# Optimization experiments

Hardware: AMD Instinct MI355X
Metric: run time of the kernel (lower is better)

## Reference

```python
import jax, jax.numpy as jnp
import numpy as np

LATENT_DIM = 8
HALF = LATENT_DIM // 2
N_BLOCKS = 3
EPS = 1e-10


def _causal_graphs(koopman):
    # koopman: [C, D, D] real. Batched eig-decomp, band-pass eigenvalues by |lam| in [0.9, 1.1],
    # equivalent to selecting stable columns/rows: V_s diag(lam_s) V_s^-1 == V diag(lam*mask) V^-1.
    lam, V = jnp.linalg.eig(koopman)            # lam: [C,D] complex, V: [C,D,D]
    Vinv = jnp.linalg.inv(V)
    lam = lam + (1e-10 + 1e-10j)
    a = jnp.abs(lam)
    mask = (a <= 1.1) & (a >= 0.9)              # [C,D]
    # fallback: if no stable eigenvalue in a group, keep all (torch.arange branch)
    mask = jnp.where(jnp.any(mask, axis=-1, keepdims=True), mask, True)
    lam_m = lam * mask.astype(lam.dtype)
    G = jnp.einsum('cij,cj,cjk->cik', V, lam_m, Vinv)
    return jnp.real(G).astype(koopman.dtype)    # [C,D,D]


def _coupling(x, cond, W0, b0, W1, b1, W2, b2):
    # Conditional affine coupling flow: x,cond [..., D]. Returns (z, logdet [...])
    logdet = jnp.zeros(x.shape[:-1], dtype=x.dtype)
    for i in range(N_BLOCKS):
        x1, x2 = x[..., :HALF], x[..., HALF:]
        if i % 2 == 1:
            x1, x2 = x2, x1
        h = jnp.concatenate([x1, cond], axis=-1)            # [..., HALF + D]
        h = jax.nn.relu(h @ W0[i] + b0[i])
        h = jax.nn.relu(h @ W1[i] + b1[i])
        o = h @ W2[i] + b2[i]                               # [..., 2*HALF]
        s = jnp.tanh(o[..., :HALF])
        t = o[..., HALF:]
        x2 = x2 * jnp.exp(s) + t
        logdet = logdet + jnp.sum(s, axis=-1)
        if i % 2 == 1:
            x1, x2 = x2, x1
        x = jnp.concatenate([x1, x2], axis=-1)
    return x, logdet


def _std_normal_logprob(z):
    # standard MVN log prob, summed over last dim
    D = z.shape[-1]
    c = jnp.asarray(0.5 * D * np.log(2.0 * np.pi), dtype=z.dtype)
    return -0.5 * jnp.sum(z * z, axis=-1) - c


def setup_inputs() -> dict:
    key = jax.random.key(0)
    ks = jax.random.split(key, 9)
    B, N, T, D, C, H = 32, 4096, 16, LATENT_DIM, 32, 64
    latent = jax.random.normal(ks[0], (B, N, T, D), dtype=jnp.float32)
    # scale so eigenvalue magnitudes cluster near ~1 (spectral radius of D x D gaussian ~ 0.35*sqrt(D))
    koopman_tilde = jax.random.normal(ks[1], (C, D, D), dtype=jnp.float32) * 0.35
    community = jax.random.normal(ks[2], (N, C), dtype=jnp.float32)
    s0 = 1.0 / np.sqrt(HALF + D)
    s1 = 1.0 / np.sqrt(H)
    W0 = jax.random.normal(ks[3], (N_BLOCKS, HALF + D, H), dtype=jnp.float32) * s0
    b0 = jnp.zeros((N_BLOCKS, H), dtype=jnp.float32)
    W1 = jax.random.normal(ks[4], (N_BLOCKS, H, H), dtype=jnp.float32) * s1
    b1 = jnp.zeros((N_BLOCKS, H), dtype=jnp.float32)
    W2 = jax.random.normal(ks[5], (N_BLOCKS, H, 2 * HALF), dtype=jnp.float32) * s1
    b2 = jnp.zeros((N_BLOCKS, 2 * HALF), dtype=jnp.float32)
    return {"latent": latent, "koopman_tilde": koopman_tilde, "community": community,
            "W0": W0, "b0": b0, "W1": W1, "b1": b1, "W2": W2, "b2": b2}


def reference(latent, koopman_tilde, community, W0, b0, W1, b1, W2, b2):
    # scale_type == 'community' branch
    community_class = jnp.argmax(community, axis=-1)        # [N], topk k=1 indices
    graphs = _causal_graphs(koopman_tilde)                  # [C, D, D]
    G_node = graphs[community_class]                        # [N, D, D] gather per node
    # dispatch/matmul/combine fused as one einsum (parent[:, class==i] = latent[:, class==i] @ G_i)
    parent = jnp.einsum('bntd,nde->bnte', latent, G_node)
    ez, logdet = _coupling(latent, parent, W0, b0, W1, b1, W2, b2)
    log_pz = _std_normal_logprob(ez) + logdet               # [B, N, T]
    return log_pz
```

## Files before the change

kernel.cpp:

```cpp
#include <hip/hip_runtime.h>
#include <hip/hip_bf16.h>

typedef __attribute__((ext_vector_type(8))) short     bf16x8;
typedef __attribute__((ext_vector_type(4))) float     f32x4;
typedef __attribute__((ext_vector_type(4))) unsigned  u32x4;

__device__ inline unsigned short bf16_rn(float x) {
  unsigned u = __float_as_uint(x);
  unsigned r = (u + 0x7FFFu + ((u >> 16) & 1u)) >> 16;
  return (unsigned short)r;
}
__device__ inline unsigned cvt_pk_bf16(float a, float b) {
  unsigned r;
  asm("v_cvt_pk_bf16_f32 %0, %1, %2" : "=v"(r) : "v"(a), "v"(b));
  return r;
}
__device__ inline void cbar() { asm volatile("" ::: "memory"); }
__device__ inline float tanh_fast(float v) {
  float vv = fminf(fmaxf(v, -15.f), 15.f);
  float e = __expf(2.f * vv);
  return (e - 1.f) * __frcp_rn(e + 1.f);
}

__global__ __launch_bounds__(256) void prologue_kernel(
    const float* __restrict__ Kt, const float* __restrict__ comm,
    const float* __restrict__ W0, const float* __restrict__ W1,
    const float* __restrict__ W2,
    float* __restrict__ Gout, int* __restrict__ cls,
    unsigned* __restrict__ wfrag)
{
  const int b = blockIdx.x;
  const int t = threadIdx.x;

  if (b < 32) {
    __shared__ double Kd[64];
    __shared__ double Pw[2][64];
    __shared__ double psum[8];
    __shared__ double coefs[9];
    __shared__ double rts[16];
    __shared__ double Gpart[64][8];

    const int tl = t & 63;
    const int row = tl >> 3, col = tl & 7;

    if (t < 64) Kd[tl] = (double)Kt[b * 64 + tl];
    __syncthreads();
    if (t < 64) Pw[0][tl] = Kd[tl];
    __syncthreads();

    int cur = 0;
    for (int p = 1; p <= 8; ++p) {
      if (t == 0) {
        double tr = 0.0;
        for (int d = 0; d < 8; ++d) tr += Pw[cur][d * 9];
        psum[p - 1] = tr;
      }
      if (p < 8 && t < 64) {
        double sacc = 0.0;
        for (int k = 0; k < 8; ++k) sacc += Pw[cur][row * 8 + k] * Kd[k * 8 + col];
        Pw[cur ^ 1][tl] = sacc;
      }
      __syncthreads();
      cur ^= 1;
    }

    if (t == 0) {
      double a[9];
      a[0] = 1.0;
      for (int k = 1; k <= 8; ++k) {
        double ssum = psum[k - 1];
        for (int i = 1; i < k; ++i) ssum += a[i] * psum[k - i - 1];
        a[k] = -ssum / (double)k;
      }
      for (int k = 0; k <= 8; ++k) coefs[k] = a[k];
    }
    __syncthreads();

    if (t < 8) {
      double a8[9];
      #pragma unroll
      for (int k = 0; k <= 8; ++k) a8[k] = coefs[k];
      double zre = 1.0, zim = 0.0;
      for (int q = 0; q <= t; ++q) {
        double t1 = zre * 0.4 - zim * 0.9;
        double t2 = zre * 0.9 + zim * 0.4;
        zre = t1; zim = t2;
      }
      for (int it = 0; it < 40; ++it) {
        double pre = a8[0], pim = 0.0;
        #pragma unroll
        for (int k = 1; k <= 8; ++k) {
          double t1 = pre * zre - pim * zim + a8[k];
          double t2 = pre * zim + pim * zre;
          pre = t1; pim = t2;
        }
        double dre = 1.0, dim = 0.0;
        for (int j = 0; j < 8; ++j) {
          double ore = __shfl(zre, j, 64);
          double oim = __shfl(zim, j, 64);
          if (j != t) {
            double sre = zre - ore, sim = zim - oim;
            double t1 = dre * sre - dim * sim;
            double t2 = dre * sim + dim * sre;
            dre = t1; dim = t2;
          }
        }
        double d2 = dre * dre + dim * dim;
        if (d2 < 1e-60) d2 = 1e-60;
        double qre = (pre * dre + pim * dim) / d2;
        double qim = (pim * dre - pre * dim) / d2;
        zre -= qre; zim -= qim;
      }
      rts[t] = zre; rts[8 + t] = zim;
    }
    __syncthreads();

    if (t < 64) {
      double lre[8], lim[8];
      #pragma unroll
      for (int j = 0; j < 8; ++j) { lre[j] = rts[j]; lim[j] = rts[8 + j]; }

      bool keep[8]; bool any = false;
      #pragma unroll
      for (int j = 0; j < 8; ++j) {
        double sre = lre[j] + 1e-10, sim = lim[j] + 1e-10;
        double amod = sqrt(sre * sre + sim * sim);
        keep[j] = (amod <= 1.1) && (amod >= 0.9);
        any = any || keep[j];
      }
      #pragma unroll
      for (int j = 0; j < 8; ++j) if (!any) keep[j] = true;

      const int r = tl >> 3, myrow = tl & 7;
      const int first = (r == 0) ? 1 : 0;
      double vre[8], vim[8];
      #pragma unroll
      for (int cc = 0; cc < 8; ++cc) {
        vre[cc] = Kd[myrow * 8 + cc] - ((myrow == cc) ? lre[first] : 0.0);
        vim[cc] = (myrow == cc) ? -lim[first] : 0.0;
      }
      #pragma unroll
      for (int j = 0; j < 8; ++j) {
        if (j == r || j == first) continue;
        double nre[8], nim[8];
        #pragma unroll
        for (int cc = 0; cc < 8; ++cc) {
          double are = 0.0, aim = 0.0;
          #pragma unroll
          for (int k = 0; k < 8; ++k) {
            double bre = Kd[k * 8 + cc] - ((k == cc) ? lre[j] : 0.0);
            double bim = (k == cc) ? -lim[j] : 0.0;
            are += vre[k] * bre - vim[k] * bim;
            aim += vre[k] * bim + vim[k] * bre;
          }
          nre[cc] = are; nim[cc] = aim;
        }
        #pragma unroll
        for (int cc = 0; cc < 8; ++cc) { vre[cc] = nre[cc]; vim[cc] = nim[cc]; }
      }

      double dre = 1.0, dim = 0.0;
      #pragma unroll
      for (int j = 0; j < 8; ++j) {
        if (j == r) continue;
        double ure = lre[r] - lre[j], uim = lim[r] - lim[j];
        double t1 = dre * ure - dim * uim;
        double t2 = dre * uim + dim * ure;
        dre = t1; dim = t2;
      }
      double numre = keep[r] ? (lre[r] + 1e-10) : 0.0;
      double numim = keep[r] ? (lim[r] + 1e-10) : 0.0;
      double dd = dre * dre + dim * dim;
      if (dd < 1e-300) dd = 1e-300;
      double cre = (numre * dre + numim * dim) / dd;
      double cim = (numim * dre - numre * dim) / dd;

      #pragma unroll
      for (int cc = 0; cc < 8; ++cc)
        Gpart[tl][cc] = cre * vre[cc] - cim * vim[cc];
    }
    __syncthreads();

    if (t < 64) {
      double sum = 0.0;
      #pragma unroll
      for (int rr = 0; rr < 8; ++rr) sum += Gpart[rr * 8 + (t >> 3)][t & 7];
      Gout[b * 64 + t] = (float)sum;
    }
    return;
  }

  if (b < 48) {
    int n = (b - 32) * 256 + t;
    if (n < 4096) {
      const float* rowp = comm + n * 32;
      float best = rowp[0];
      int bi = 0;
      #pragma unroll
      for (int c = 1; c < 32; ++c) {
        float v = rowp[c];
        if (v > best) { best = v; bi = c; }
      }
      cls[n] = bi;
    }
    return;
  }

  {
    int gid = (b - 48) * 256 + t;
    if (gid >= 42 * 64) return;
    int fid = gid >> 6, lane = gid & 63;
    int i = fid / 14, fl = fid % 14;
    int c = lane & 15, g = lane >> 4;

    unsigned short vals[8];
    #pragma unroll
    for (int j = 0; j < 8; ++j) {
      float v = 0.f;
      if (fl < 4) {
        int nb = fl;
        int k = 8 * g + j;
        if (k < 12) v = W0[i * 768 + k * 64 + 16 * nb + c];
      } else if (fl < 12) {
        int q = fl - 4; int kb = q >> 2, nb = q & 3;
        int k = 32 * kb + 16 * ((j >> 2) & 1) + 4 * g + 2 * ((j >> 1) & 1) + (j & 1);
        v = W1[i * 4096 + k * 64 + 16 * nb + c];
      } else {
        int kb = fl - 12;
        int k = 32 * kb + 16 * ((j >> 2) & 1) + 4 * g + 2 * ((j >> 1) & 1) + (j & 1);
        if (c < 8) v = W2[i * 512 + k * 8 + c];
      }
      vals[j] = bf16_rn(v);
    }
    u32x4 o;
    #pragma unroll
    for (int tt = 0; tt < 4; ++tt)
      o[tt] = (unsigned)vals[2 * tt] | ((unsigned)vals[2 * tt + 1] << 16);
    *(u32x4*)(wfrag + fid * 256 + lane * 4) = o;
  }
}

#define SPB 256

__global__ __launch_bounds__(256, 3) void causal_mfma_kernel(
    const float* __restrict__ latent, const float* __restrict__ graphs,
    const int* __restrict__ cls, const unsigned* __restrict__ wfrag,
    const float* __restrict__ b0, const float* __restrict__ b1,
    const float* __restrict__ b2, float* __restrict__ out)
{
  __shared__ char LW[4][4096];

  const int t = threadIdx.x;
  const int lane = t & 63;
  const int w = t >> 6;
  const int c = lane & 15;
  const int g = lane >> 4;
  const int s = blockIdx.x * SPB + t;
  char* my = LW[w];

  float x[8];
  {
    const float4 xa = *(const float4*)(latent + (size_t)s * 8);
    const float4 xb = *(const float4*)(latent + (size_t)s * 8 + 4);
    x[0] = xa.x; x[1] = xa.y; x[2] = xa.z; x[3] = xa.w;
    x[4] = xb.x; x[5] = xb.y; x[6] = xb.z; x[7] = xb.w;
  }
  unsigned parP0, parP1;
  u32x4 hi4;
  {
    float par[8];
    const int n = (s >> 4) & 4095;
    const float* G = graphs + cls[n] * 64;
    #pragma unroll
    for (int e = 0; e < 8; ++e) par[e] = 0.f;
    #pragma unroll
    for (int d = 0; d < 8; ++d) {
      const float xd = x[d];
      const float4 g0 = *(const float4*)(G + d * 8);
      const float4 g1 = *(const float4*)(G + d * 8 + 4);
      par[0] += xd * g0.x; par[1] += xd * g0.y; par[2] += xd * g0.z; par[3] += xd * g0.w;
      par[4] += xd * g1.x; par[5] += xd * g1.y; par[6] += xd * g1.z; par[7] += xd * g1.w;
    }
    parP0 = cvt_pk_bf16(par[0], par[1]);
    parP1 = cvt_pk_bf16(par[2], par[3]);
    hi4[0] = cvt_pk_bf16(par[4], par[5]);
    hi4[1] = cvt_pk_bf16(par[6], par[7]);
    hi4[2] = 0u; hi4[3] = 0u;
  }

  const int ssw = (lane >> 2) & 3;
  char* a_u0 = my + lane * 64 + ((0 ^ ssw) << 4);
  char* a_u1 = my + lane * 64 + ((1 ^ ssw) << 4);
  {
    const u32x4 z = {0u, 0u, 0u, 0u};
    *(u32x4*)(my + lane * 64 + ((2 ^ ssw) << 4)) = z;
    *(u32x4*)(my + lane * 64 + ((3 ^ ssw) << 4)) = z;
  }
  const int gsw = g ^ (c >> 2);
  char* a_b0 = my + (c)      * 64 + (gsw << 4);
  char* a_b1 = my + (16 + c) * 64 + (gsw << 4);
  char* a_b2 = my + (32 + c) * 64 + (gsw << 4);
  char* a_b3 = my + (48 + c) * 64 + (gsw << 4);

  float logdet = 0.f;

  #pragma unroll
  for (int i = 0; i < 3; ++i) {
    const int in0 = (i & 1) ? 4 : 0;
    const int tr0 = (i & 1) ? 0 : 4;
    const char* wbase = (const char*)wfrag + (size_t)(i * 14) * 1024 + lane * 16;

    {
      u32x4 lo4;
      lo4[0] = cvt_pk_bf16(x[in0], x[in0 + 1]);
      lo4[1] = cvt_pk_bf16(x[in0 + 2], x[in0 + 3]);
      lo4[2] = parP0; lo4[3] = parP1;
      *(u32x4*)a_u0 = lo4;
      *(u32x4*)a_u1 = hi4;
    }
    cbar();

    u32x4 B1[4];
    B1[0] = *(const u32x4*)a_b0;
    B1[1] = *(const u32x4*)a_b1;
    B1[2] = *(const u32x4*)a_b2;
    B1[3] = *(const u32x4*)a_b3;

    u32x4 B2k0[4], B2k1[4];
    {
      f32x4 a0[4], a1[4];
      bf16x8 A0 = *(const bf16x8*)(wbase + 0 * 1024);
      bf16x8 A1 = *(const bf16x8*)(wbase + 1 * 1024);
      f32x4 bv0 = *(const f32x4*)(b0 + i * 64 + 0 * 16 + g * 4);
      f32x4 bv1 = *(const f32x4*)(b0 + i * 64 + 1 * 16 + g * 4);
      #pragma unroll
      for (int mb = 0; mb < 4; ++mb)
        a0[mb] = __builtin_amdgcn_mfma_f32_16x16x32_bf16(
            A0, __builtin_bit_cast(bf16x8, B1[mb]), bv0, 0, 0, 0);
      #pragma unroll
      for (int mb = 0; mb < 4; ++mb)
        a1[mb] = __builtin_amdgcn_mfma_f32_16x16x32_bf16(
            A1, __builtin_bit_cast(bf16x8, B1[mb]), bv1, 0, 0, 0);
      #pragma unroll
      for (int mb = 0; mb < 4; ++mb) {
        B2k0[mb] = u32x4{cvt_pk_bf16(fmaxf(a0[mb][0], 0.f), fmaxf(a0[mb][1], 0.f)),
                         cvt_pk_bf16(fmaxf(a0[mb][2], 0.f), fmaxf(a0[mb][3], 0.f)),
                         cvt_pk_bf16(fmaxf(a1[mb][0], 0.f), fmaxf(a1[mb][1], 0.f)),
                         cvt_pk_bf16(fmaxf(a1[mb][2], 0.f), fmaxf(a1[mb][3], 0.f))};
      }
    }
    {
      f32x4 a0[4], a1[4];
      bf16x8 A0 = *(const bf16x8*)(wbase + 2 * 1024);
      bf16x8 A1 = *(const bf16x8*)(wbase + 3 * 1024);
      f32x4 bv0 = *(const f32x4*)(b0 + i * 64 + 2 * 16 + g * 4);
      f32x4 bv1 = *(const f32x4*)(b0 + i * 64 + 3 * 16 + g * 4);
      #pragma unroll
      for (int mb = 0; mb < 4; ++mb)
        a0[mb] = __builtin_amdgcn_mfma_f32_16x16x32_bf16(
            A0, __builtin_bit_cast(bf16x8, B1[mb]), bv0, 0, 0, 0);
      #pragma unroll
      for (int mb = 0; mb < 4; ++mb)
        a1[mb] = __builtin_amdgcn_mfma_f32_16x16x32_bf16(
            A1, __builtin_bit_cast(bf16x8, B1[mb]), bv1, 0, 0, 0);
      #pragma unroll
      for (int mb = 0; mb < 4; ++mb) {
        B2k1[mb] = u32x4{cvt_pk_bf16(fmaxf(a0[mb][0], 0.f), fmaxf(a0[mb][1], 0.f)),
                         cvt_pk_bf16(fmaxf(a0[mb][2], 0.f), fmaxf(a0[mb][3], 0.f)),
                         cvt_pk_bf16(fmaxf(a1[mb][0], 0.f), fmaxf(a1[mb][1], 0.f)),
                         cvt_pk_bf16(fmaxf(a1[mb][2], 0.f), fmaxf(a1[mb][3], 0.f))};
      }
    }

    u32x4 B3k0[4], B3k1[4];
    {
      f32x4 a0[4], a1[4];
      bf16x8 Ak0n0 = *(const bf16x8*)(wbase + (4 + 0) * 1024);
      bf16x8 Ak0n1 = *(const bf16x8*)(wbase + (4 + 1) * 1024);
      bf16x8 Ak1n0 = *(const bf16x8*)(wbase + (8 + 0) * 1024);
      bf16x8 Ak1n1 = *(const bf16x8*)(wbase + (8 + 1) * 1024);
      f32x4 bv0 = *(const f32x4*)(b1 + i * 64 + 0 * 16 + g * 4);
      f32x4 bv1 = *(const f32x4*)(b1 + i * 64 + 1 * 16 + g * 4);
      #pragma unroll
      for (int mb = 0; mb < 4; ++mb) {
        a0[mb] = __builtin_amdgcn_mfma_f32_16x16x32_bf16(
            Ak0n0, __builtin_bit_cast(bf16x8, B2k0[mb]), bv0, 0, 0, 0);
        a0[mb] = __builtin_amdgcn_mfma_f32_16x16x32_bf16(
            Ak1n0, __builtin_bit_cast(bf16x8, B2k1[mb]), a0[mb], 0, 0, 0);
      }
      #pragma unroll
      for (int mb = 0; mb < 4; ++mb) {
        a1[mb] = __builtin_amdgcn_mfma_f32_16x16x32_bf16(
            Ak0n1, __builtin_bit_cast(bf16x8, B2k0[mb]), bv1, 0, 0, 0);
        a1[mb] = __builtin_amdgcn_mfma_f32_16x16x32_bf16(
            Ak1n1, __builtin_bit_cast(bf16x8, B2k1[mb]), a1[mb], 0, 0, 0);
      }
      #pragma unroll
      for (int mb = 0; mb < 4; ++mb) {
        B3k0[mb] = u32x4{cvt_pk_bf16(fmaxf(a0[mb][0], 0.f), fmaxf(a0[mb][1], 0.f)),
                         cvt_pk_bf16(fmaxf(a0[mb][2], 0.f), fmaxf(a0[mb][3], 0.f)),
                         cvt_pk_bf16(fmaxf(a1[mb][0], 0.f), fmaxf(a1[mb][1], 0.f)),
                         cvt_pk_bf16(fmaxf(a1[mb][2], 0.f), fmaxf(a1[mb][3], 0.f))};
      }
    }
    {
      f32x4 a0[4], a1[4];
      bf16x8 Ak0n2 = *(const bf16x8*)(wbase + (4 + 2) * 1024);
      bf16x8 Ak0n3 = *(const bf16x8*)(wbase + (4 + 3) * 1024);
      bf16x8 Ak1n2 = *(const bf16x8*)(wbase + (8 + 2) * 1024);
      bf16x8 Ak1n3 = *(const bf16x8*)(wbase + (8 + 3) * 1024);
      f32x4 bv0 = *(const f32x4*)(b1 + i * 64 + 2 * 16 + g * 4);
      f32x4 bv1 = *(const f32x4*)(b1 + i * 64 + 3 * 16 + g * 4);
      #pragma unroll
      for (int mb = 0; mb < 4; ++mb) {
        a0[mb] = __builtin_amdgcn_mfma_f32_16x16x32_bf16(
            Ak0n2, __builtin_bit_cast(bf16x8, B2k0[mb]), bv0, 0, 0, 0);
        a0[mb] = __builtin_amdgcn_mfma_f32_16x16x32_bf16(
            Ak1n2, __builtin_bit_cast(bf16x8, B2k1[mb]), a0[mb], 0, 0, 0);
      }
      #pragma unroll
      for (int mb = 0; mb < 4; ++mb) {
        a1[mb] = __builtin_amdgcn_mfma_f32_16x16x32_bf16(
            Ak0n3, __builtin_bit_cast(bf16x8, B2k0[mb]), bv1, 0, 0, 0);
        a1[mb] = __builtin_amdgcn_mfma_f32_16x16x32_bf16(
            Ak1n3, __builtin_bit_cast(bf16x8, B2k1[mb]), a1[mb], 0, 0, 0);
      }
      #pragma unroll
      for (int mb = 0; mb < 4; ++mb) {
        B3k1[mb] = u32x4{cvt_pk_bf16(fmaxf(a0[mb][0], 0.f), fmaxf(a0[mb][1], 0.f)),
                         cvt_pk_bf16(fmaxf(a0[mb][2], 0.f), fmaxf(a0[mb][3], 0.f)),
                         cvt_pk_bf16(fmaxf(a1[mb][0], 0.f), fmaxf(a1[mb][1], 0.f)),
                         cvt_pk_bf16(fmaxf(a1[mb][2], 0.f), fmaxf(a1[mb][3], 0.f))};
      }
    }

    f32x4 acc3[4];
    {
      bf16x8 A0 = *(const bf16x8*)(wbase + 12 * 1024);
      bf16x8 A1 = *(const bf16x8*)(wbase + 13 * 1024);
      f32x4 z = {0.f, 0.f, 0.f, 0.f};
      f32x4 bC2 = (g < 2) ? *(const f32x4*)(b2 + i * 8 + g * 4) : z;
      #pragma unroll
      for (int mb = 0; mb < 4; ++mb) {
        f32x4 tmp = __builtin_amdgcn_mfma_f32_16x16x32_bf16(
            A0, __builtin_bit_cast(bf16x8, B3k0[mb]), bC2, 0, 0, 0);
        acc3[mb] = __builtin_amdgcn_mfma_f32_16x16x32_bf16(
            A1, __builtin_bit_cast(bf16x8, B3k1[mb]), tmp, 0, 0, 0);
      }
    }

    *(u32x4*)a_b0 = __builtin_bit_cast(u32x4, acc3[0]);
    *(u32x4*)a_b1 = __builtin_bit_cast(u32x4, acc3[1]);
    *(u32x4*)a_b2 = __builtin_bit_cast(u32x4, acc3[2]);
    *(u32x4*)a_b3 = __builtin_bit_cast(u32x4, acc3[3]);
    cbar();

    {
      u32x4 o0 = *(const u32x4*)a_u0;
      u32x4 o1 = *(const u32x4*)a_u1;
      float sv0 = tanh_fast(__uint_as_float(o0[0]));
      float sv1 = tanh_fast(__uint_as_float(o0[1]));
      float sv2 = tanh_fast(__uint_as_float(o0[2]));
      float sv3 = tanh_fast(__uint_as_float(o0[3]));
      x[tr0 + 0] = x[tr0 + 0] * __expf(sv0) + __uint_as_float(o1[0]);
      x[tr0 + 1] = x[tr0 + 1] * __expf(sv1) + __uint_as_float(o1[1]);
      x[tr0 + 2] = x[tr0 + 2] * __expf(sv2) + __uint_as_float(o1[2]);
      x[tr0 + 3] = x[tr0 + 3] * __expf(sv3) + __uint_as_float(o1[3]);
      logdet += sv0 + sv1 + sv2 + sv3;
    }
  }

  float ss = 0.f;
  #pragma unroll
  for (int q = 0; q < 8; ++q) ss += x[q] * x[q];
  out[s] = -0.5f * ss - 7.3515082656373810f + logdet;
}

extern "C" void kernel_launch(void* const* d_in, const int* in_sizes, int n_in,
                              void* d_out, int out_size, void* d_ws, size_t ws_size,
                              hipStream_t stream) {
  const float* latent  = (const float*)d_in[0];
  const float* koopman = (const float*)d_in[1];
  const float* comm    = (const float*)d_in[2];
  const float* W0      = (const float*)d_in[3];
  const float* b0      = (const float*)d_in[4];
  const float* W1      = (const float*)d_in[5];
  const float* b1      = (const float*)d_in[6];
  const float* W2      = (const float*)d_in[7];
  const float* b2      = (const float*)d_in[8];
  float* out = (float*)d_out;

  float*    graphs_ws = (float*)d_ws;
  int*      cls_ws    = (int*)((char*)d_ws + 8192);
  unsigned* wfrag_ws  = (unsigned*)((char*)d_ws + 24576);

  prologue_kernel<<<59, 256, 0, stream>>>(
      koopman, comm, W0, W1, W2, graphs_ws, cls_ws, wfrag_ws);

  const int total = 32 * 4096 * 16;
  causal_mfma_kernel<<<total / SPB, SPB, 0, stream>>>(
      latent, graphs_ws, cls_ws, wfrag_ws, b0, b1, b2, out);
}
```

Baseline: 160.9 us.

## Stage MLP weight fragments and biases in LDS, shrink per-wave exchange buffer

Each block now copies all 42 bf16 weight fragments and the three bias vectors into shared memory once, then reads A-operands and biases from LDS instead of global memory inside the unrolled coupling loop. The per-wave exchange buffer is halved by dropping the zero-padded K half (upper lanes now zero their B operand in registers instead of reading zeros from LDS), and swizzling is removed. Compiler-only barriers are replaced with explicit lgkmcnt waits. Costs are about 50KB more LDS per block, which may reduce occupancy below the requested 3 blocks per CU, a block-wide sync, and possible bank conflicts from the unswizzled layout.

New measurement: 154.7 us. 3.9% less time.

```diff
diff --git a/kernel.cpp b/kernel.cpp
--- a/kernel.cpp
+++ b/kernel.cpp
@@ -15,7 +15,9 @@
   asm("v_cvt_pk_bf16_f32 %0, %1, %2" : "=v"(r) : "v"(a), "v"(b));
   return r;
 }
-__device__ inline void cbar() { asm volatile("" ::: "memory"); }
+__device__ inline void wfence() {
+  asm volatile("s_waitcnt lgkmcnt(0)" ::: "memory");
+}
 __device__ inline float tanh_fast(float v) {
   float vv = fminf(fmaxf(v, -15.f), 15.f);
   float e = __expf(2.f * vv);
@@ -248,7 +250,9 @@
     const float* __restrict__ b0, const float* __restrict__ b1,
     const float* __restrict__ b2, float* __restrict__ out)
 {
-  __shared__ char LW[4][4096];
+  __shared__ unsigned wsh[42 * 256];
+  __shared__ float    bsh[408];
+  __shared__ char     ex[4][2048];
 
   const int t = threadIdx.x;
   const int lane = t & 63;
@@ -256,7 +260,17 @@
   const int c = lane & 15;
   const int g = lane >> 4;
   const int s = blockIdx.x * SPB + t;
-  char* my = LW[w];
+  char* my = ex[w];
+
+  #pragma unroll
+  for (int q = 0; q < 11; ++q) {
+    int idx = q * 256 + t;
+    if (idx < 42 * 64)
+      *(u32x4*)(wsh + idx * 4) = *(const u32x4*)(wfrag + idx * 4);
+  }
+  for (int idx = t; idx < 408; idx += 256) {
+    bsh[idx] = (idx < 192) ? b0[idx] : (idx < 384) ? b1[idx - 192] : b2[idx - 384];
+  }
 
   float x[8];
   {
@@ -288,19 +302,14 @@
     hi4[2] = 0u; hi4[3] = 0u;
   }
 
-  const int ssw = (lane >> 2) & 3;
-  char* a_u0 = my + lane * 64 + ((0 ^ ssw) << 4);
-  char* a_u1 = my + lane * 64 + ((1 ^ ssw) << 4);
-  {
-    const u32x4 z = {0u, 0u, 0u, 0u};
-    *(u32x4*)(my + lane * 64 + ((2 ^ ssw) << 4)) = z;
-    *(u32x4*)(my + lane * 64 + ((3 ^ ssw) << 4)) = z;
-  }
-  const int gsw = g ^ (c >> 2);
-  char* a_b0 = my + (c)      * 64 + (gsw << 4);
-  char* a_b1 = my + (16 + c) * 64 + (gsw << 4);
-  char* a_b2 = my + (32 + c) * 64 + (gsw << 4);
-  char* a_b3 = my + (48 + c) * 64 + (gsw << 4);
+  __syncthreads();
+
+  const char* wl = (const char*)wsh + lane * 16;
+  char* a_u  = my + lane * 32;
+  char* a_b0 = my + (c)      * 32 + g * 16;
+  char* a_b1 = my + (16 + c) * 32 + g * 16;
+  char* a_b2 = my + (32 + c) * 32 + g * 16;
+  char* a_b3 = my + (48 + c) * 32 + g * 16;
 
   float logdet = 0.f;
 
@@ -308,31 +317,35 @@
   for (int i = 0; i < 3; ++i) {
     const int in0 = (i & 1) ? 4 : 0;
     const int tr0 = (i & 1) ? 0 : 4;
-    const char* wbase = (const char*)wfrag + (size_t)(i * 14) * 1024 + lane * 16;
+    const char* wbase = wl + (size_t)(i * 14) * 1024;
 
     {
       u32x4 lo4;
       lo4[0] = cvt_pk_bf16(x[in0], x[in0 + 1]);
       lo4[1] = cvt_pk_bf16(x[in0 + 2], x[in0 + 3]);
       lo4[2] = parP0; lo4[3] = parP1;
-      *(u32x4*)a_u0 = lo4;
-      *(u32x4*)a_u1 = hi4;
-    }
-    cbar();
+      wfence();
+      *(u32x4*)a_u = lo4;
+      *(u32x4*)(a_u + 16) = hi4;
+      wfence();
+    }
 
     u32x4 B1[4];
-    B1[0] = *(const u32x4*)a_b0;
-    B1[1] = *(const u32x4*)a_b1;
-    B1[2] = *(const u32x4*)a_b2;
-    B1[3] = *(const u32x4*)a_b3;
+    {
+      u32x4 z = {0u, 0u, 0u, 0u};
+      B1[0] = (g < 2) ? *(const u32x4*)a_b0 : z;
+      B1[1] = (g < 2) ? *(const u32x4*)a_b1 : z;
+      B1[2] = (g < 2) ? *(const u32x4*)a_b2 : z;
+      B1[3] = (g < 2) ? *(const u32x4*)a_b3 : z;
+    }
 
     u32x4 B2k0[4], B2k1[4];
     {
       f32x4 a0[4], a1[4];
       bf16x8 A0 = *(const bf16x8*)(wbase + 0 * 1024);
       bf16x8 A1 = *(const bf16x8*)(wbase + 1 * 1024);
-      f32x4 bv0 = *(const f32x4*)(b0 + i * 64 + 0 * 16 + g * 4);
-      f32x4 bv1 = *(const f32x4*)(b0 + i * 64 + 1 * 16 + g * 4);
+      f32x4 bv0 = *(const f32x4*)(bsh + i * 64 + 0 * 16 + g * 4);
+      f32x4 bv1 = *(const f32x4*)(bsh + i * 64 + 1 * 16 + g * 4);
       #pragma unroll
       for (int mb = 0; mb < 4; ++mb)
         a0[mb] = __builtin_amdgcn_mfma_f32_16x16x32_bf16(
@@ -353,8 +366,8 @@
       f32x4 a0[4], a1[4];
       bf16x8 A0 = *(const bf16x8*)(wbase + 2 * 1024);
       bf16x8 A1 = *(const bf16x8*)(wbase + 3 * 1024);
-      f32x4 bv0 = *(const f32x4*)(b0 + i * 64 + 2 * 16 + g * 4);
-      f32x4 bv1 = *(const f32x4*)(b0 + i * 64 + 3 * 16 + g * 4);
+      f32x4 bv0 = *(const f32x4*)(bsh + i * 64 + 2 * 16 + g * 4);
+      f32x4 bv1 = *(const f32x4*)(bsh + i * 64 + 3 * 16 + g * 4);
       #pragma unroll
       for (int mb = 0; mb < 4; ++mb)
         a0[mb] = __builtin_amdgcn_mfma_f32_16x16x32_bf16(
@@ -379,8 +392,8 @@
       bf16x8 Ak0n1 = *(const bf16x8*)(wbase + (4 + 1) * 1024);
       bf16x8 Ak1n0 = *(const bf16x8*)(wbase + (8 + 0) * 1024);
       bf16x8 Ak1n1 = *(const bf16x8*)(wbase + (8 + 1) * 1024);
-      f32x4 bv0 = *(const f32x4*)(b1 + i * 64 + 0 * 16 + g * 4);
-      f32x4 bv1 = *(const f32x4*)(b1 + i * 64 + 1 * 16 + g * 4);
+      f32x4 bv0 = *(const f32x4*)(bsh + 192 + i * 64 + 0 * 16 + g * 4);
+      f32x4 bv1 = *(const f32x4*)(bsh + 192 + i * 64 + 1 * 16 + g * 4);
       #pragma unroll
       for (int mb = 0; mb < 4; ++mb) {
         a0[mb] = __builtin_amdgcn_mfma_f32_16x16x32_bf16(
@@ -409,8 +422,8 @@
       bf16x8 Ak0n3 = *(const bf16x8*)(wbase + (4 + 3) * 1024);
       bf16x8 Ak1n2 = *(const bf16x8*)(wbase + (8 + 2) * 1024);
       bf16x8 Ak1n3 = *(const bf16x8*)(wbase + (8 + 3) * 1024);
-      f32x4 bv0 = *(const f32x4*)(b1 + i * 64 + 2 * 16 + g * 4);
-      f32x4 bv1 = *(const f32x4*)(b1 + i * 64 + 3 * 16 + g * 4);
+      f32x4 bv0 = *(const f32x4*)(bsh + 192 + i * 64 + 2 * 16 + g * 4);
+      f32x4 bv1 = *(const f32x4*)(bsh + 192 + i * 64 + 3 * 16 + g * 4);
       #pragma unroll
       for (int mb = 0; mb < 4; ++mb) {
         a0[mb] = __builtin_amdgcn_mfma_f32_16x16x32_bf16(
@@ -439,7 +452,7 @@
       bf16x8 A0 = *(const bf16x8*)(wbase + 12 * 1024);
       bf16x8 A1 = *(const bf16x8*)(wbase + 13 * 1024);
       f32x4 z = {0.f, 0.f, 0.f, 0.f};
-      f32x4 bC2 = (g < 2) ? *(const f32x4*)(b2 + i * 8 + g * 4) : z;
+      f32x4 bC2 = (g < 2) ? *(const f32x4*)(bsh + 384 + i * 8 + g * 4) : z;
       #pragma unroll
       for (int mb = 0; mb < 4; ++mb) {
         f32x4 tmp = __builtin_amdgcn_mfma_f32_16x16x32_bf16(
@@ -449,15 +462,18 @@
       }
     }
 
-    *(u32x4*)a_b0 = __builtin_bit_cast(u32x4, acc3[0]);
-    *(u32x4*)a_b1 = __builtin_bit_cast(u32x4, acc3[1]);
-    *(u32x4*)a_b2 = __builtin_bit_cast(u32x4, acc3[2]);
-    *(u32x4*)a_b3 = __builtin_bit_cast(u32x4, acc3[3]);
-    cbar();
-
-    {
-      u32x4 o0 = *(const u32x4*)a_u0;
-      u32x4 o1 = *(const u32x4*)a_u1;
+    wfence();
+    if (g < 2) {
+      *(u32x4*)a_b0 = __builtin_bit_cast(u32x4, acc3[0]);
+      *(u32x4*)a_b1 = __builtin_bit_cast(u32x4, acc3[1]);
+      *(u32x4*)a_b2 = __builtin_bit_cast(u32x4, acc3[2]);
+      *(u32x4*)a_b3 = __builtin_bit_cast(u32x4, acc3[3]);
+    }
+    wfence();
+
+    {
+      u32x4 o0 = *(const u32x4*)a_u;
+      u32x4 o1 = *(const u32x4*)(a_u + 16);
       float sv0 = tanh_fast(__uint_as_float(o0[0]));
       float sv1 = tanh_fast(__uint_as_float(o0[1]));
       float sv2 = tanh_fast(__uint_as_float(o0[2]));
```

## Stage MLP weight fragments and biases in shared memory per block

Applied to the files above, without the earlier changes.

Each block now cooperatively copies the pre-packed bf16 weight fragments (42 KB) and all biases into LDS, then reads MFMA operands from LDS instead of global/L2 on every use. The launch-bounds occupancy hint drops from 3 to 2 blocks per CU to accommodate the larger LDS footprint, and the tanh reciprocal uses the raw hardware rcp builtin. The staging adds a per-block global copy and a __syncthreads, and the lower occupancy may reduce latency hiding.

New measurement: 165.6 us. +2.9%, slower.

```diff
diff --git a/kernel.cpp b/kernel.cpp
--- a/kernel.cpp
+++ b/kernel.cpp
@@ -19,7 +19,7 @@
 __device__ inline float tanh_fast(float v) {
   float vv = fminf(fmaxf(v, -15.f), 15.f);
   float e = __expf(2.f * vv);
-  return (e - 1.f) * __frcp_rn(e + 1.f);
+  return (e - 1.f) * __builtin_amdgcn_rcpf(e + 1.f);
 }
 
 __global__ __launch_bounds__(256) void prologue_kernel(
@@ -242,13 +242,15 @@
 
 #define SPB 256
 
-__global__ __launch_bounds__(256, 3) void causal_mfma_kernel(
+__global__ __launch_bounds__(256, 2) void causal_mfma_kernel(
     const float* __restrict__ latent, const float* __restrict__ graphs,
     const int* __restrict__ cls, const unsigned* __restrict__ wfrag,
     const float* __restrict__ b0, const float* __restrict__ b1,
     const float* __restrict__ b2, float* __restrict__ out)
 {
-  __shared__ char LW[4][4096];
+  __shared__ unsigned wsh[42 * 256];
+  __shared__ float    bsh[408];
+  __shared__ char     ex[4][4096];
 
   const int t = threadIdx.x;
   const int lane = t & 63;
@@ -256,7 +258,31 @@
   const int c = lane & 15;
   const int g = lane >> 4;
   const int s = blockIdx.x * SPB + t;
-  char* my = LW[w];
+  char* my = ex[w];
+
+  #pragma unroll
+  for (int q = 0; q < 11; ++q) {
+    int idx = q * 256 + t;
+    if (idx < 42 * 64)
+      *(u32x4*)(wsh + idx * 4) = *(const u32x4*)(wfrag + idx * 4);
+  }
+  for (int idx = t; idx < 408; idx += 256) {
+    bsh[idx] = (idx < 192) ? b0[idx] : (idx < 384) ? b1[idx - 192] : b2[idx - 384];
+  }
+
+  const int ssw = (lane >> 2) & 3;
+  char* a_u0 = my + lane * 64 + ((0 ^ ssw) << 4);
+  char* a_u1 = my + lane * 64 + ((1 ^ ssw) << 4);
+  {
+    const u32x4 z = {0u, 0u, 0u, 0u};
+    *(u32x4*)(my + lane * 64 + ((2 ^ ssw) << 4)) = z;
+    *(u32x4*)(my + lane * 64 + ((3 ^ ssw) << 4)) = z;
+  }
+  const int gsw = g ^ (c >> 2);
+  char* a_b0 = my + (c)      * 64 + (gsw << 4);
+  char* a_b1 = my + (16 + c) * 64 + (gsw << 4);
+  char* a_b2 = my + (32 + c) * 64 + (gsw << 4);
+  char* a_b3 = my + (48 + c) * 64 + (gsw << 4);
 
   float x[8];
   {
@@ -288,19 +314,9 @@
     hi4[2] = 0u; hi4[3] = 0u;
   }
 
-  const int ssw = (lane >> 2) & 3;
-  char* a_u0 = my + lane * 64 + ((0 ^ ssw) << 4);
-  char* a_u1 = my + lane * 64 + ((1 ^ ssw) << 4);
-  {
-    const u32x4 z = {0u, 0u, 0u, 0u};
-    *(u32x4*)(my + lane * 64 + ((2 ^ ssw) << 4)) = z;
-    *(u32x4*)(my + lane * 64 + ((3 ^ ssw) << 4)) = z;
-  }
-  const int gsw = g ^ (c >> 2);
-  char* a_b0 = my + (c)      * 64 + (gsw << 4);
-  char* a_b1 = my + (16 + c) * 64 + (gsw << 4);
-  char* a_b2 = my + (32 + c) * 64 + (gsw << 4);
-  char* a_b3 = my + (48 + c) * 64 + (gsw << 4);
+  __syncthreads();
+
+  const char* wl = (const char*)wsh + lane * 16;
 
   float logdet = 0.f;
 
@@ -308,7 +324,7 @@
   for (int i = 0; i < 3; ++i) {
     const int in0 = (i & 1) ? 4 : 0;
     const int tr0 = (i & 1) ? 0 : 4;
-    const char* wbase = (const char*)wfrag + (size_t)(i * 14) * 1024 + lane * 16;
+    const char* wbase = wl + (size_t)(i * 14) * 1024;
 
     {
       u32x4 lo4;
@@ -331,8 +347,8 @@
       f32x4 a0[4], a1[4];
       bf16x8 A0 = *(const bf16x8*)(wbase + 0 * 1024);
       bf16x8 A1 = *(const bf16x8*)(wbase + 1 * 1024);
-      f32x4 bv0 = *(const f32x4*)(b0 + i * 64 + 0 * 16 + g * 4);
-      f32x4 bv1 = *(const f32x4*)(b0 + i * 64 + 1 * 16 + g * 4);
+      f32x4 bv0 = *(const f32x4*)(bsh + i * 64 + 0 * 16 + g * 4);
+      f32x4 bv1 = *(const f32x4*)(bsh + i * 64 + 1 * 16 + g * 4);
       #pragma unroll
       for (int mb = 0; mb < 4; ++mb)
         a0[mb] = __builtin_amdgcn_mfma_f32_16x16x32_bf16(
@@ -353,8 +369,8 @@
       f32x4 a0[4], a1[4];
       bf16x8 A0 = *(const bf16x8*)(wbase + 2 * 1024);
       bf16x8 A1 = *(const bf16x8*)(wbase + 3 * 1024);
-      f32x4 bv0 = *(const f32x4*)(b0 + i * 64 + 2 * 16 + g * 4);
-      f32x4 bv1 = *(const f32x4*)(b0 + i * 64 + 3 * 16 + g * 4);
+      f32x4 bv0 = *(const f32x4*)(bsh + i * 64 + 2 * 16 + g * 4);
+      f32x4 bv1 = *(const f32x4*)(bsh + i * 64 + 3 * 16 + g * 4);
       #pragma unroll
       for (int mb = 0; mb < 4; ++mb)
         a0[mb] = __builtin_amdgcn_mfma_f32_16x16x32_bf16(
@@ -379,8 +395,8 @@
       bf16x8 Ak0n1 = *(const bf16x8*)(wbase + (4 + 1) * 1024);
       bf16x8 Ak1n0 = *(const bf16x8*)(wbase + (8 + 0) * 1024);
       bf16x8 Ak1n1 = *(const bf16x8*)(wbase + (8 + 1) * 1024);
-      f32x4 bv0 = *(const f32x4*)(b1 + i * 64 + 0 * 16 + g * 4);
-      f32x4 bv1 = *(const f32x4*)(b1 + i * 64 + 1 * 16 + g * 4);
+      f32x4 bv0 = *(const f32x4*)(bsh + 192 + i * 64 + 0 * 16 + g * 4);
+      f32x4 bv1 = *(const f32x4*)(bsh + 192 + i * 64 + 1 * 16 + g * 4);
       #pragma unroll
       for (int mb = 0; mb < 4; ++mb) {
         a0[mb] = __builtin_amdgcn_mfma_f32_16x16x32_bf16(
@@ -409,8 +425,8 @@
       bf16x8 Ak0n3 = *(const bf16x8*)(wbase + (4 + 3) * 1024);
       bf16x8 Ak1n2 = *(const bf16x8*)(wbase + (8 + 2) * 1024);
       bf16x8 Ak1n3 = *(const bf16x8*)(wbase + (8 + 3) * 1024);
-      f32x4 bv0 = *(const f32x4*)(b1 + i * 64 + 2 * 16 + g * 4);
-      f32x4 bv1 = *(const f32x4*)(b1 + i * 64 + 3 * 16 + g * 4);
+      f32x4 bv0 = *(const f32x4*)(bsh + 192 + i * 64 + 2 * 16 + g * 4);
+      f32x4 bv1 = *(const f32x4*)(bsh + 192 + i * 64 + 3 * 16 + g * 4);
       #pragma unroll
       for (int mb = 0; mb < 4; ++mb) {
         a0[mb] = __builtin_amdgcn_mfma_f32_16x16x32_bf16(
@@ -439,7 +455,7 @@
       bf16x8 A0 = *(const bf16x8*)(wbase + 12 * 1024);
       bf16x8 A1 = *(const bf16x8*)(wbase + 13 * 1024);
       f32x4 z = {0.f, 0.f, 0.f, 0.f};
-      f32x4 bC2 = (g < 2) ? *(const f32x4*)(b2 + i * 8 + g * 4) : z;
+      f32x4 bC2 = (g < 2) ? *(const f32x4*)(bsh + 384 + i * 8 + g * 4) : z;
       #pragma unroll
       for (int mb = 0; mb < 4; ++mb) {
         f32x4 tmp = __builtin_amdgcn_mfma_f32_16x16x32_bf16(
```
